# Kernel optimization log

Hardware: AMD Instinct MI355X
Metric: run time of the kernel (lower is better)

Reference implementation:

```python
import jax, jax.numpy as jnp
import numpy as np

SPLIT_SHAPE = (16, 16, 16, 16)  # per-variable state counts; joint space = 65536
NUM_CLASSES = 100
STABLE = 1e-6


def setup_inputs() -> dict:
    key = jax.random.key(0)
    k1, k2 = jax.random.split(key)
    B = 1024
    logits = jax.random.normal(k1, (B, sum(SPLIT_SHAPE)), dtype=jnp.float32)
    labels = jax.random.randint(k2, (B,), 0, NUM_CLASSES)
    y_true = jax.nn.one_hot(labels, NUM_CLASSES, dtype=jnp.float32)
    return {"logits": logits, "y_true": y_true}


def reference(logits, y_true):
    B = logits.shape[0]
    # split logits into per-variable blocks and softmax each -> P(Ak|Xi)
    splits = np.cumsum(SPLIT_SHAPE)[:-1]
    variables = [jax.nn.softmax(p, axis=-1) for p in jnp.split(logits, splits, axis=-1)]
    # joint sample space via iterative outer products: [B, s1, ..., sN]
    joint = variables[0]
    for v in variables[1:]:
        joint = jnp.einsum('b...,ba->b...a', joint, v)
    flat = joint.reshape(B, -1)  # [B, J], J = prod(SPLIT_SHAPE)
    # observation: numerator/denominator counts (fresh recorder, first call)
    num_y_joint = jnp.einsum('bj,by->yj', flat, y_true)  # [Y, J]
    num_joint = jnp.sum(flat, axis=0)                     # [J]
    prob_y_joint = jnp.clip(
        jnp.maximum(num_y_joint, STABLE) / jnp.maximum(num_joint, STABLE), 0.0, 1.0)
    # inference: posterior P^A(Yi|Xi)
    probs = jnp.einsum('yj,bj->by', prob_y_joint, flat)  # [B, Y]
    return probs
```

## Files before the change

kernel.cpp:

```cpp
#include <hip/hip_runtime.h>
#include <hip/hip_bf16.h>

#define EPS 1e-6f

typedef float f32x4 __attribute__((ext_vector_type(4)));
typedef __bf16 bf16x8 __attribute__((ext_vector_type(8)));
typedef short short8 __attribute__((ext_vector_type(8)));

static __device__ __forceinline__ short bf16bits(float x) {
    __hip_bfloat16 h = __float2bfloat16(x);
    short s;
    __builtin_memcpy(&s, &h, 2);
    return s;
}
static __device__ __forceinline__ void bsplit(float x, short& h, short& l) {
    __hip_bfloat16 hb = __float2bfloat16(x);
    __builtin_memcpy(&h, &hb, 2);
    float hf = __bfloat162float(hb);
    __hip_bfloat16 lb = __float2bfloat16(x - hf);
    __builtin_memcpy(&l, &lb, 2);
}

static __device__ __forceinline__ bf16x8 gload16(const short* p) {
    bf16x8 r;
    asm volatile("global_load_dwordx4 %0, %1, off"
                 : "=&v"(r) : "v"(p) : "memory");
    return r;
}
#define WAITV(N)                                                   \
    do {                                                           \
        asm volatile("s_waitcnt vmcnt(" #N ")" ::: "memory");      \
        __builtin_amdgcn_sched_barrier(0);                         \
    } while (0)

__global__ __launch_bounds__(256) void kA(const float* __restrict__ logits,
                                          const float* __restrict__ y_true,
                                          float* __restrict__ P23,
                                          float* __restrict__ P01,
                                          float* __restrict__ P01T,
                                          short* __restrict__ P23s_hi,
                                          int* __restrict__ label,
                                          float* __restrict__ numjoint) {
    __shared__ float row[64];
    int b = blockIdx.x, t = threadIdx.x;
    if (t < 64) {
        float x = logits[b * 64 + t];
        float m = x;
        for (int mk = 8; mk >= 1; mk >>= 1) m = fmaxf(m, __shfl_xor(m, mk, 16));
        float e = __expf(x - m);
        float s = e;
        for (int mk = 8; mk >= 1; mk >>= 1) s += __shfl_xor(s, mk, 16);
        row[t] = e / s;
    }
    if (t >= 128 && t < 228) {
        int y = t - 128;
        if (y_true[b * 100 + y] > 0.5f) label[b] = y;
    }
    if (t < 64) numjoint[b * 64 + t] = 0.f;
    __syncthreads();
    int hi = t >> 4, lo = t & 15;
    float v01 = row[hi] * row[16 + lo];
    float v23 = row[32 + hi] * row[48 + lo];
    P01[b * 256 + t] = v01;
    P01T[t * 1024 + b] = v01;
    P23[b * 256 + t] = v23;
    int ts = t ^ ((b & 7) << 3);
    P23s_hi[b * 256 + ts] = bf16bits(v23);
}

__global__ __launch_bounds__(256, 4) void kSNJ(const float* __restrict__ P01T,
                                               const float* __restrict__ P23,
                                               const int* __restrict__ label,
                                               int* __restrict__ bidx,
                                               int* __restrict__ off_g,
                                               float* __restrict__ numjoint) {
    int t = threadIdx.x;
    int bid = blockIdx.x;

    if (bid == 256) {
        __shared__ int lab[1024];
        __shared__ unsigned bm[101 * 32];
        __shared__ int hist[101];
        __shared__ int offs[101];
        for (int i = t; i < 1024; i += 256) lab[i] = label[i];
        if (t < 101) hist[t] = 0;
        for (int i = t; i < 101 * 32; i += 256) bm[i] = 0u;
        __syncthreads();
        for (int i = t; i < 1024; i += 256) {
            int my = lab[i];
            atomicAdd(&hist[my], 1);
            atomicOr(&bm[my * 32 + (i >> 5)], 1u << (i & 31));
        }
        __syncthreads();
        if (t == 0) {
            int s = 0;
            for (int y = 0; y < 101; ++y) { offs[y] = s; s += hist[y]; }
        }
        __syncthreads();
        for (int i = t; i < 1024; i += 256) {
            int my = lab[i];
            int w = i >> 5;
            int rank = 0;
            for (int q = 0; q < 32; ++q)
                if (q < w) rank += __popc(bm[my * 32 + q]);
            rank += __popc(bm[my * 32 + w] & ((1u << (i & 31)) - 1u));
            bidx[offs[my] + rank] = i;
        }
        if (t <= 100) off_g[t] = offs[t];
        return;
    }

    __shared__ short Bh[4 * 64 * 8];
    __shared__ short Bl[4 * 64 * 8];
    int ub = (bid & 3) << 6;
    int tb = ((bid >> 2) & 3) << 6;
    int koff = (bid >> 4) << 6;
    int lane = t & 63, w = t >> 6;
    int l15 = lane & 15, l4 = lane >> 4;

    const float* pa = P01T + (size_t)(ub + w * 16 + l15) * 1024 + koff + (l4 << 3);
    int sr = t >> 3, sc = (t & 7) << 3;

    const f32x4 zero4 = {0.f, 0.f, 0.f, 0.f};
    f32x4 acc0 = zero4, acc1 = zero4, acc2 = zero4, acc3 = zero4;

    #pragma unroll
    for (int kc = 0; kc < 2; ++kc) {
        __syncthreads();
        {
            const float* pb = P23 + (size_t)(koff + kc * 32 + sr) * 256 + tb + sc;
            #pragma unroll
            for (int q = 0; q < 8; ++q) {
                short h, l;
                bsplit(pb[q], h, l);
                int tcl = sc + q;
                int ad = (((tcl >> 4) << 6) + (tcl & 15) + ((sr >> 3) << 4)) * 8 + (sr & 7);
                Bh[ad] = h; Bl[ad] = l;
            }
        }
        __syncthreads();
        union { short8 s; bf16x8 b; } Ah, Al;
        #pragma unroll
        for (int q = 0; q < 8; ++q) {
            short h, l;
            bsplit(pa[kc * 32 + q], h, l);
            Ah.s[q] = h; Al.s[q] = l;
        }
        {
            bf16x8 bh0 = *(const bf16x8*)(Bh + (lane) * 8);
            bf16x8 bl0 = *(const bf16x8*)(Bl + (lane) * 8);
            bf16x8 bh1 = *(const bf16x8*)(Bh + (64 + lane) * 8);
            bf16x8 bl1 = *(const bf16x8*)(Bl + (64 + lane) * 8);
            bf16x8 bh2 = *(const bf16x8*)(Bh + (128 + lane) * 8);
            bf16x8 bl2 = *(const bf16x8*)(Bl + (128 + lane) * 8);
            bf16x8 bh3 = *(const bf16x8*)(Bh + (192 + lane) * 8);
            bf16x8 bl3 = *(const bf16x8*)(Bl + (192 + lane) * 8);
            acc0 = __builtin_amdgcn_mfma_f32_16x16x32_bf16(Ah.b, bh0, acc0, 0, 0, 0);
            acc0 = __builtin_amdgcn_mfma_f32_16x16x32_bf16(Ah.b, bl0, acc0, 0, 0, 0);
            acc0 = __builtin_amdgcn_mfma_f32_16x16x32_bf16(Al.b, bh0, acc0, 0, 0, 0);
            acc1 = __builtin_amdgcn_mfma_f32_16x16x32_bf16(Ah.b, bh1, acc1, 0, 0, 0);
            acc1 = __builtin_amdgcn_mfma_f32_16x16x32_bf16(Ah.b, bl1, acc1, 0, 0, 0);
            acc1 = __builtin_amdgcn_mfma_f32_16x16x32_bf16(Al.b, bh1, acc1, 0, 0, 0);
            acc2 = __builtin_amdgcn_mfma_f32_16x16x32_bf16(Ah.b, bh2, acc2, 0, 0, 0);
            acc2 = __builtin_amdgcn_mfma_f32_16x16x32_bf16(Ah.b, bl2, acc2, 0, 0, 0);
            acc2 = __builtin_amdgcn_mfma_f32_16x16x32_bf16(Al.b, bh2, acc2, 0, 0, 0);
            acc3 = __builtin_amdgcn_mfma_f32_16x16x32_bf16(Ah.b, bh3, acc3, 0, 0, 0);
            acc3 = __builtin_amdgcn_mfma_f32_16x16x32_bf16(Ah.b, bl3, acc3, 0, 0, 0);
            acc3 = __builtin_amdgcn_mfma_f32_16x16x32_bf16(Al.b, bh3, acc3, 0, 0, 0);
        }
    }
    #pragma unroll
    for (int n = 0; n < 4; ++n) {
        f32x4 a = (n == 0) ? acc0 : (n == 1) ? acc1 : (n == 2) ? acc2 : acc3;
        #pragma unroll
        for (int r = 0; r < 4; ++r) {
            int u = ub + w * 16 + (l4 << 2) + r;
            int tc = tb + (n << 4) + l15;
            atomicAdd(&numjoint[u * 256 + tc], a[r]);
        }
    }
}

__global__ __launch_bounds__(256, 2) void kY(const float* __restrict__ P01,
                                             const float* __restrict__ P23,
                                             const int* __restrict__ bidx,
                                             const int* __restrict__ off_g,
                                             const float* __restrict__ numjoint,
                                             short* __restrict__ pyF) {
    __shared__ short Bh[8 * 64 * 8];
    __shared__ short Bl[8 * 64 * 8];
    __shared__ short ct[4][16 * 128];
    __shared__ float aStage[32][258];
    __shared__ int sbidx[32];
    int y = blockIdx.x >> 1;
    int th = blockIdx.x & 1;
    int t = threadIdx.x;
    int lane = t & 63, w = t >> 6;
    int l15 = lane & 15, l4 = lane >> 4;
    int yt = y >> 4, yl = y & 15;

    if (y >= 100) {
        short8 z = {0, 0, 0, 0, 0, 0, 0, 0};
        #pragma unroll
        for (int ut = 0; ut < 4; ++ut)
            #pragma unroll
            for (int rep = 0; rep < 4; ++rep) {
                int c = (rep << 6) + lane;
                int ul = c >> 4, t8 = (c & 15) << 3;
                int u = (w << 6) + (ut << 4) + ul;
                int j0 = u * 256 + (th << 7) + t8;
                size_t sa = ((size_t)((j0 >> 5) * 8 + yt) * 64 + yl + (((j0 >> 3) & 3) << 4)) * 8;
                *(short8*)(pyF + sa) = z;
            }
        return;
    }

    int off = off_g[y];
    int n = off_g[y + 1] - off;
    int nk = (n + 31) >> 5;

    const f32x4 zero4 = {0.f, 0.f, 0.f, 0.f};
    f32x4 acc[4][8];
    #pragma unroll
    for (int a = 0; a < 4; ++a)
        #pragma unroll
        for (int b = 0; b < 8; ++b) acc[a][b] = zero4;

    int sr = t >> 3, sc = (t & 7) << 3;

    #pragma unroll 1
    for (int kc = 0; kc < nk; ++kc) {
        __syncthreads();
        if (t < 32) {
            int idx = off + kc * 32 + t;
            sbidx[t] = bidx[(idx < 1024) ? idx : 1023];
        }
        __syncthreads();
        for (int it = 0; it < 32; ++it)
            aStage[it][t] = P01[sbidx[it] * 256 + t];
        #pragma unroll
        for (int rep = 0; rep < 2; ++rep) {
            int tl0 = (rep << 6) + sc;
            int row = kc * 32 + sr;
            float vals[8];
            if (row < n) {
                const float* pb = P23 + (size_t)sbidx[sr] * 256 + (th << 7) + tl0;
                #pragma unroll
                for (int q = 0; q < 8; ++q) vals[q] = pb[q];
            } else {
                #pragma unroll
                for (int q = 0; q < 8; ++q) vals[q] = 0.f;
            }
            #pragma unroll
            for (int q = 0; q < 8; ++q) {
                short h, l;
                bsplit(vals[q], h, l);
                int tl = tl0 + q;
                int ad = (((tl >> 4) << 6) + (tl & 15) + ((sr >> 3) << 4)) * 8 + (sr & 7);
                Bh[ad] = h; Bl[ad] = l;
            }
        }
        __syncthreads();
        #pragma unroll
        for (int ut = 0; ut < 4; ++ut) {
            union { short8 s; bf16x8 b; } Ah, Al;
            #pragma unroll
            for (int q = 0; q < 8; ++q) {
                short h, l;
                bsplit(aStage[(l4 << 3) + q][(w << 6) + (ut << 4) + l15], h, l);
                Ah.s[q] = h; Al.s[q] = l;
            }
            #pragma unroll
            for (int tt = 0; tt < 8; ++tt) {
                bf16x8 bh = *(const bf16x8*)(Bh + ((tt << 6) + lane) * 8);
                bf16x8 bl = *(const bf16x8*)(Bl + ((tt << 6) + lane) * 8);
                acc[ut][tt] = __builtin_amdgcn_mfma_f32_16x16x32_bf16(Ah.b, bh, acc[ut][tt], 0, 0, 0);
                acc[ut][tt] = __builtin_amdgcn_mfma_f32_16x16x32_bf16(Ah.b, bl, acc[ut][tt], 0, 0, 0);
                acc[ut][tt] = __builtin_amdgcn_mfma_f32_16x16x32_bf16(Al.b, bh, acc[ut][tt], 0, 0, 0);
            }
        }
    }

    #pragma unroll
    for (int ut = 0; ut < 4; ++ut) {
        #pragma unroll
        for (int tt = 0; tt < 8; ++tt) {
            #pragma unroll
            for (int r = 0; r < 4; ++r) {
                int u = (w << 6) + (ut << 4) + (l4 << 2) + r;
                int tg = (th << 7) + (tt << 4) + l15;
                float nj = numjoint[u * 256 + tg];
                float q = fminf(fmaxf(acc[ut][tt][r], EPS) / fmaxf(nj, EPS), 1.0f);
                ct[w][((l4 << 2) + r) * 128 + (tt << 4) + l15] = bf16bits(q);
            }
        }
        asm volatile("s_waitcnt lgkmcnt(0)" ::: "memory");
        __builtin_amdgcn_sched_barrier(0);
        #pragma unroll
        for (int rep = 0; rep < 4; ++rep) {
            int c = (rep << 6) + lane;
            int ul = c >> 4, t8 = (c & 15) << 3;
            short8 v = *(const short8*)(ct[w] + ul * 128 + t8);
            int u = (w << 6) + (ut << 4) + ul;
            int j0 = u * 256 + (th << 7) + t8;
            size_t sa = ((size_t)((j0 >> 5) * 8 + yt) * 64 + yl + (((j0 >> 3) & 3) << 4)) * 8;
            *(short8*)(pyF + sa) = v;
        }
        asm volatile("s_waitcnt lgkmcnt(0)" ::: "memory");
        __builtin_amdgcn_sched_barrier(0);
    }
}

__global__ __launch_bounds__(512, 2) void kC(const short* __restrict__ P23s_hi,
                                             const float* __restrict__ P01T,
                                             const short* __restrict__ pyF,
                                             float* __restrict__ part) {
    __shared__ short Ahi[64 * 256];
    __shared__ float p01s[8 * 64];
    int t = threadIdx.x;
    int bb = blockIdx.x >> 5, uspl = blockIdx.x & 31;
    int bbase = bb << 6;
    int u0 = uspl << 3;

    #pragma unroll
    for (int r = 0; r < 4; ++r) {
        int c = r * 512 + t;
        *(short8*)(Ahi + c * 8) = *(const short8*)(P23s_hi + bbase * 256 + c * 8);
    }
    p01s[t] = P01T[(u0 + (t >> 6)) * 1024 + bbase + (t & 63)];
    __syncthreads();

    int lane = t & 63;
    int wave = t >> 6;
    int wb = wave >> 2, wy = wave & 3;
    int l15 = lane & 15, l4 = lane >> 4;
    int hi8 = l4 << 3;

    int rowA0 = wb * 32 + l15;
    int swz = (rowA0 & 7) << 3;
    const short* pA0h = Ahi + rowA0 * 256;
    const short* pA1h = pA0h + 16 * 256;

    const short* pf = pyF + (size_t)(uspl * 64 * 8 + wy * 2) * 512 + lane * 8;
    int y0 = wy * 32 + l15;

    const f32x4 zero4 = {0.f, 0.f, 0.f, 0.f};
    f32x4 P00 = zero4, P01v = zero4, P10 = zero4, P11 = zero4;
    bf16x8 W0, W1, X0, X1, Y0, Y1, Z0, Z1;

#define COMPUTE(CUR0, CUR1, KS)                                                  \
    {                                                                            \
        int aoff = ((KS) * 32 + hi8) ^ swz;                                      \
        bf16x8 a0h = *(const bf16x8*)(pA0h + aoff);                              \
        bf16x8 a1h = *(const bf16x8*)(pA1h + aoff);                              \
        f32x4 c00 = ((KS) == 0) ? zero4 : Q00;                                   \
        f32x4 c01 = ((KS) == 0) ? zero4 : Q01;                                   \
        f32x4 c10 = ((KS) == 0) ? zero4 : Q10;                                   \
        f32x4 c11 = ((KS) == 0) ? zero4 : Q11;                                   \
        c00 = __builtin_amdgcn_mfma_f32_16x16x32_bf16(a0h, CUR0, c00, 0, 0, 0);  \
        c10 = __builtin_amdgcn_mfma_f32_16x16x32_bf16(a1h, CUR0, c10, 0, 0, 0);  \
        c01 = __builtin_amdgcn_mfma_f32_16x16x32_bf16(a0h, CUR1, c01, 0, 0, 0);  \
        c11 = __builtin_amdgcn_mfma_f32_16x16x32_bf16(a1h, CUR1, c11, 0, 0, 0);  \
        Q00 = c00; Q01 = c01; Q10 = c10; Q11 = c11;                              \
    }
#define STEP(CUR0, CUR1, NXT0, NXT1, KS, S3)    \
    NXT0 = gload16(pf + (S3) * 4096);           \
    NXT1 = gload16(pf + (S3) * 4096 + 512);     \
    WAITV(6);                                   \
    COMPUTE(CUR0, CUR1, KS)

    {
        W0 = gload16(pf);        W1 = gload16(pf + 512);
        X0 = gload16(pf + 4096); X1 = gload16(pf + 4096 + 512);
        Y0 = gload16(pf + 8192); Y1 = gload16(pf + 8192 + 512);
    }

    #pragma unroll 1
    for (int uu = 0; uu < 7; ++uu) {
        int s0 = uu * 8;
        f32x4 Q00, Q01, Q10, Q11;
        STEP(W0, W1, Z0, Z1, 0, s0 + 3)
        STEP(X0, X1, W0, W1, 1, s0 + 4)
        STEP(Y0, Y1, X0, X1, 2, s0 + 5)
        STEP(Z0, Z1, Y0, Y1, 3, s0 + 6)
        STEP(W0, W1, Z0, Z1, 4, s0 + 7)
        STEP(X0, X1, W0, W1, 5, s0 + 8)
        STEP(Y0, Y1, X0, X1, 6, s0 + 9)
        STEP(Z0, Z1, Y0, Y1, 7, s0 + 10)
        f32x4 pv0 = *(const f32x4*)(p01s + uu * 64 + wb * 32 + (l4 << 2));
        f32x4 pv1 = *(const f32x4*)(p01s + uu * 64 + wb * 32 + 16 + (l4 << 2));
        P00 += pv0 * Q00; P01v += pv0 * Q01;
        P10 += pv1 * Q10; P11 += pv1 * Q11;
    }
    {
        f32x4 Q00, Q01, Q10, Q11;
        STEP(W0, W1, Z0, Z1, 0, 59)
        STEP(X0, X1, W0, W1, 1, 60)
        STEP(Y0, Y1, X0, X1, 2, 61)
        STEP(Z0, Z1, Y0, Y1, 3, 62)
        STEP(W0, W1, Z0, Z1, 4, 63)
        WAITV(4); COMPUTE(X0, X1, 5)
        WAITV(2); COMPUTE(Y0, Y1, 6)
        WAITV(0); COMPUTE(Z0, Z1, 7)
        f32x4 pv0 = *(const f32x4*)(p01s + 7 * 64 + wb * 32 + (l4 << 2));
        f32x4 pv1 = *(const f32x4*)(p01s + 7 * 64 + wb * 32 + 16 + (l4 << 2));
        P00 += pv0 * Q00; P01v += pv0 * Q01;
        P10 += pv1 * Q10; P11 += pv1 * Q11;
    }
#undef STEP
#undef COMPUTE

    size_t pbase = (size_t)uspl * 128 * 1024;
    {
        int bg0 = bbase + wb * 32 + (l4 << 2);
        int bg1 = bg0 + 16;
        *(f32x4*)(part + pbase + (size_t)y0 * 1024 + bg0) = P00;
        *(f32x4*)(part + pbase + (size_t)y0 * 1024 + bg1) = P10;
        *(f32x4*)(part + pbase + (size_t)(y0 + 16) * 1024 + bg0) = P01v;
        *(f32x4*)(part + pbase + (size_t)(y0 + 16) * 1024 + bg1) = P11;
    }
}

__global__ __launch_bounds__(256) void kD(const float* __restrict__ part,
                                          float* __restrict__ out) {
    int t = threadIdx.x;
    int y = blockIdx.x >> 2;
    int b = ((blockIdx.x & 3) << 8) + t;
    float s = 0.f;
    for (int q = 0; q < 32; ++q)
        s += part[(((size_t)q * 128 + y) << 10) + b];
    out[(size_t)b * 100 + y] = s;
}

extern "C" void kernel_launch(void* const* d_in, const int* in_sizes, int n_in,
                              void* d_out, int out_size, void* d_ws, size_t ws_size,
                              hipStream_t stream) {
    const float* logits = (const float*)d_in[0];
    const float* y_true = (const float*)d_in[1];
    float* out = (float*)d_out;

    char* ws = (char*)d_ws;
    float* P01      = (float*)(ws);
    float* P23      = (float*)(ws + (1u << 20));
    float* P01T     = (float*)(ws + (2u << 20));
    short* P23s_hi  = (short*)(ws + (3u << 20));
    int*   lab      = (int*)(ws + (4u << 20));
    int*   bidx     = (int*)(ws + (4u << 20) + 4096);
    int*   off_g    = (int*)(ws + (4u << 20) + 8192);
    short* pyF      = (short*)(ws + (8u << 20));
    float* numjoint = (float*)(ws + (24u << 20));
    float* part     = (float*)(ws + (40u << 20));

    kA<<<1024, 256, 0, stream>>>(logits, y_true, P23, P01, P01T, P23s_hi, lab, numjoint);
    kSNJ<<<257, 256, 0, stream>>>(P01T, P23, lab, bidx, off_g, numjoint);
    kY<<<256, 256, 0, stream>>>(P01, P23, bidx, off_g, numjoint, pyF);
    kC<<<512, 512, 0, stream>>>(P23s_hi, P01T, pyF, part);
    kD<<<400, 256, 0, stream>>>(part, out);
}
```

Measured before the change: 75.95 us.

## Give each kC wave all 64 batch rows so streamed pyF tiles are reused across them

The kC block is halved from 8 to 4 waves, and each wave now computes all 64 batch rows (four 16-row A tiles) against its 32 y columns, instead of two waves splitting the rows. Each global pyF fragment load now feeds 8 MFMAs instead of 4, halving the global/L2 read traffic for pyF. In exchange there are twice the accumulator registers and fewer waves per block, which may reduce occupancy and latency hiding.

```diff
diff --git a/kernel.cpp b/kernel.cpp
--- a/kernel.cpp
+++ b/kernel.cpp
@@ -311,41 +311,43 @@
     }
 }
 
-__global__ __launch_bounds__(512, 2) void kC(const short* __restrict__ P23s_hi,
+__global__ __launch_bounds__(256, 2) void kC(const short* __restrict__ P23s_hi,
                                              const float* __restrict__ P01T,
                                              const short* __restrict__ pyF,
                                              float* __restrict__ part) {
     __shared__ short Ahi[64 * 256];
-    __shared__ float p01s[8 * 64];
+    __shared__ float p01s[512];
     int t = threadIdx.x;
     int bb = blockIdx.x >> 5, uspl = blockIdx.x & 31;
     int bbase = bb << 6;
     int u0 = uspl << 3;
 
     #pragma unroll
-    for (int r = 0; r < 4; ++r) {
-        int c = r * 512 + t;
+    for (int r = 0; r < 8; ++r) {
+        int c = r * 256 + t;
         *(short8*)(Ahi + c * 8) = *(const short8*)(P23s_hi + bbase * 256 + c * 8);
     }
     p01s[t] = P01T[(u0 + (t >> 6)) * 1024 + bbase + (t & 63)];
+    p01s[256 + t] = P01T[(u0 + 4 + (t >> 6)) * 1024 + bbase + (t & 63)];
     __syncthreads();
 
     int lane = t & 63;
-    int wave = t >> 6;
-    int wb = wave >> 2, wy = wave & 3;
+    int wy = t >> 6;
     int l15 = lane & 15, l4 = lane >> 4;
     int hi8 = l4 << 3;
 
-    int rowA0 = wb * 32 + l15;
-    int swz = (rowA0 & 7) << 3;
-    const short* pA0h = Ahi + rowA0 * 256;
+    int swz = (l15 & 7) << 3;
+    const short* pA0h = Ahi + l15 * 256;
     const short* pA1h = pA0h + 16 * 256;
-
-    const short* pf = pyF + (size_t)(uspl * 64 * 8 + wy * 2) * 512 + lane * 8;
+    const short* pA2h = pA0h + 32 * 256;
+    const short* pA3h = pA0h + 48 * 256;
+
+    const short* pf = pyF + (size_t)(uspl * 512 + wy * 2) * 512 + lane * 8;
     int y0 = wy * 32 + l15;
 
     const f32x4 zero4 = {0.f, 0.f, 0.f, 0.f};
     f32x4 P00 = zero4, P01v = zero4, P10 = zero4, P11 = zero4;
+    f32x4 P20 = zero4, P21 = zero4, P30 = zero4, P31 = zero4;
     bf16x8 W0, W1, X0, X1, Y0, Y1, Z0, Z1;
 
 #define COMPUTE(CUR0, CUR1, KS)                                                  \
@@ -353,15 +355,26 @@
         int aoff = ((KS) * 32 + hi8) ^ swz;                                      \
         bf16x8 a0h = *(const bf16x8*)(pA0h + aoff);                              \
         bf16x8 a1h = *(const bf16x8*)(pA1h + aoff);                              \
+        bf16x8 a2h = *(const bf16x8*)(pA2h + aoff);                              \
+        bf16x8 a3h = *(const bf16x8*)(pA3h + aoff);                              \
         f32x4 c00 = ((KS) == 0) ? zero4 : Q00;                                   \
         f32x4 c01 = ((KS) == 0) ? zero4 : Q01;                                   \
         f32x4 c10 = ((KS) == 0) ? zero4 : Q10;                                   \
         f32x4 c11 = ((KS) == 0) ? zero4 : Q11;                                   \
+        f32x4 c20 = ((KS) == 0) ? zero4 : Q20;                                   \
+        f32x4 c21 = ((KS) == 0) ? zero4 : Q21;                                   \
+        f32x4 c30 = ((KS) == 0) ? zero4 : Q30;                                   \
+        f32x4 c31 = ((KS) == 0) ? zero4 : Q31;                                   \
         c00 = __builtin_amdgcn_mfma_f32_16x16x32_bf16(a0h, CUR0, c00, 0, 0, 0);  \
         c10 = __builtin_amdgcn_mfma_f32_16x16x32_bf16(a1h, CUR0, c10, 0, 0, 0);  \
+        c20 = __builtin_amdgcn_mfma_f32_16x16x32_bf16(a2h, CUR0, c20, 0, 0, 0);  \
+        c30 = __builtin_amdgcn_mfma_f32_16x16x32_bf16(a3h, CUR0, c30, 0, 0, 0);  \
         c01 = __builtin_amdgcn_mfma_f32_16x16x32_bf16(a0h, CUR1, c01, 0, 0, 0);  \
         c11 = __builtin_amdgcn_mfma_f32_16x16x32_bf16(a1h, CUR1, c11, 0, 0, 0);  \
+        c21 = __builtin_amdgcn_mfma_f32_16x16x32_bf16(a2h, CUR1, c21, 0, 0, 0);  \
+        c31 = __builtin_amdgcn_mfma_f32_16x16x32_bf16(a3h, CUR1, c31, 0, 0, 0);  \
         Q00 = c00; Q01 = c01; Q10 = c10; Q11 = c11;                              \
+        Q20 = c20; Q21 = c21; Q30 = c30; Q31 = c31;                              \
     }
 #define STEP(CUR0, CUR1, NXT0, NXT1, KS, S3)    \
     NXT0 = gload16(pf + (S3) * 4096);           \
@@ -378,7 +391,7 @@
     #pragma unroll 1
     for (int uu = 0; uu < 7; ++uu) {
         int s0 = uu * 8;
-        f32x4 Q00, Q01, Q10, Q11;
+        f32x4 Q00, Q01, Q10, Q11, Q20, Q21, Q30, Q31;
         STEP(W0, W1, Z0, Z1, 0, s0 + 3)
         STEP(X0, X1, W0, W1, 1, s0 + 4)
         STEP(Y0, Y1, X0, X1, 2, s0 + 5)
@@ -387,13 +400,17 @@
         STEP(X0, X1, W0, W1, 5, s0 + 8)
         STEP(Y0, Y1, X0, X1, 6, s0 + 9)
         STEP(Z0, Z1, Y0, Y1, 7, s0 + 10)
-        f32x4 pv0 = *(const f32x4*)(p01s + uu * 64 + wb * 32 + (l4 << 2));
-        f32x4 pv1 = *(const f32x4*)(p01s + uu * 64 + wb * 32 + 16 + (l4 << 2));
+        f32x4 pv0 = *(const f32x4*)(p01s + uu * 64 + (l4 << 2));
+        f32x4 pv1 = *(const f32x4*)(p01s + uu * 64 + 16 + (l4 << 2));
+        f32x4 pv2 = *(const f32x4*)(p01s + uu * 64 + 32 + (l4 << 2));
+        f32x4 pv3 = *(const f32x4*)(p01s + uu * 64 + 48 + (l4 << 2));
         P00 += pv0 * Q00; P01v += pv0 * Q01;
         P10 += pv1 * Q10; P11 += pv1 * Q11;
+        P20 += pv2 * Q20; P21 += pv2 * Q21;
+        P30 += pv3 * Q30; P31 += pv3 * Q31;
     }
     {
-        f32x4 Q00, Q01, Q10, Q11;
+        f32x4 Q00, Q01, Q10, Q11, Q20, Q21, Q30, Q31;
         STEP(W0, W1, Z0, Z1, 0, 59)
         STEP(X0, X1, W0, W1, 1, 60)
         STEP(Y0, Y1, X0, X1, 2, 61)
@@ -402,22 +419,31 @@
         WAITV(4); COMPUTE(X0, X1, 5)
         WAITV(2); COMPUTE(Y0, Y1, 6)
         WAITV(0); COMPUTE(Z0, Z1, 7)
-        f32x4 pv0 = *(const f32x4*)(p01s + 7 * 64 + wb * 32 + (l4 << 2));
-        f32x4 pv1 = *(const f32x4*)(p01s + 7 * 64 + wb * 32 + 16 + (l4 << 2));
+        f32x4 pv0 = *(const f32x4*)(p01s + 7 * 64 + (l4 << 2));
+        f32x4 pv1 = *(const f32x4*)(p01s + 7 * 64 + 16 + (l4 << 2));
+        f32x4 pv2 = *(const f32x4*)(p01s + 7 * 64 + 32 + (l4 << 2));
+        f32x4 pv3 = *(const f32x4*)(p01s + 7 * 64 + 48 + (l4 << 2));
         P00 += pv0 * Q00; P01v += pv0 * Q01;
         P10 += pv1 * Q10; P11 += pv1 * Q11;
+        P20 += pv2 * Q20; P21 += pv2 * Q21;
+        P30 += pv3 * Q30; P31 += pv3 * Q31;
     }
 #undef STEP
 #undef COMPUTE
 
     size_t pbase = (size_t)uspl * 128 * 1024;
     {
-        int bg0 = bbase + wb * 32 + (l4 << 2);
-        int bg1 = bg0 + 16;
-        *(f32x4*)(part + pbase + (size_t)y0 * 1024 + bg0) = P00;
-        *(f32x4*)(part + pbase + (size_t)y0 * 1024 + bg1) = P10;
-        *(f32x4*)(part + pbase + (size_t)(y0 + 16) * 1024 + bg0) = P01v;
-        *(f32x4*)(part + pbase + (size_t)(y0 + 16) * 1024 + bg1) = P11;
+        int bg0 = bbase + (l4 << 2);
+        size_t r0 = pbase + (size_t)y0 * 1024;
+        size_t r1 = pbase + (size_t)(y0 + 16) * 1024;
+        *(f32x4*)(part + r0 + bg0)      = P00;
+        *(f32x4*)(part + r0 + bg0 + 16) = P10;
+        *(f32x4*)(part + r0 + bg0 + 32) = P20;
+        *(f32x4*)(part + r0 + bg0 + 48) = P30;
+        *(f32x4*)(part + r1 + bg0)      = P01v;
+        *(f32x4*)(part + r1 + bg0 + 16) = P11;
+        *(f32x4*)(part + r1 + bg0 + 32) = P21;
+        *(f32x4*)(part + r1 + bg0 + 48) = P31;
     }
 }
 
@@ -454,6 +480,6 @@
     kA<<<1024, 256, 0, stream>>>(logits, y_true, P23, P01, P01T, P23s_hi, lab, numjoint);
     kSNJ<<<257, 256, 0, stream>>>(P01T, P23, lab, bidx, off_g, numjoint);
     kY<<<256, 256, 0, stream>>>(P01, P23, bidx, off_g, numjoint, pyF);
-    kC<<<512, 512, 0, stream>>>(P23s_hi, P01T, pyF, part);
+    kC<<<512, 256, 0, stream>>>(P23s_hi, P01T, pyF, part);
     kD<<<400, 256, 0, stream>>>(part, out);
 }
```

New measurement: 70.55 us. 1.08x faster.
